# Performance work log

Hardware: AMD Instinct MI355X
Metric: run time of the kernel (lower is better)

The kernel has to match this reference:

```python
import jax, jax.numpy as jnp
import numpy as np

N_NODES = 50000
N_EDGES = 1000000
N_GRAPHS = 256
ORIG = 92
ATOM = 64
NBR = 41
EPS = 1e-5


def _bn_train(h, gamma, beta):
    # BatchNorm1d in training mode: batch stats, biased variance
    mu = h.mean(axis=0)
    var = jnp.var(h, axis=0)
    return (h - mu) * jax.lax.rsqrt(var + EPS) * gamma + beta


def setup_inputs() -> dict:
    key = jax.random.key(0)
    ks = jax.random.split(key, 16)
    inp = {
        "x": jax.random.normal(ks[0], (N_NODES, ORIG), dtype=jnp.float32),
        "edge_attr": jax.random.normal(ks[1], (N_EDGES, NBR), dtype=jnp.float32),
        "lower_f": jax.random.normal(ks[2], (N_NODES, ATOM), dtype=jnp.float32),
        "edge_index": jax.random.randint(ks[3], (2, N_EDGES), 0, N_NODES, dtype=jnp.int32),
        "batch": jnp.sort(jax.random.randint(ks[4], (N_NODES,), 0, N_GRAPHS, dtype=jnp.int32)),
        # params
        "emb_W": jax.random.normal(ks[5], (ORIG, ATOM), dtype=jnp.float32) / np.sqrt(ORIG),
        "emb_b": jnp.zeros((ATOM,), dtype=jnp.float32),
        "fc_W": jax.random.normal(ks[6], (2 * ATOM + NBR, 2 * ATOM), dtype=jnp.float32) / np.sqrt(2 * ATOM + NBR),
        "fc_b": jnp.zeros((2 * ATOM,), dtype=jnp.float32),
        "bn1_g": jnp.ones((2 * ATOM,), dtype=jnp.float32),
        "bn1_b": jnp.zeros((2 * ATOM,), dtype=jnp.float32),
        "bn2_g": jnp.ones((ATOM,), dtype=jnp.float32),
        "bn2_b": jnp.zeros((ATOM,), dtype=jnp.float32),
        "att_W": jax.random.normal(ks[7], (ATOM, 1), dtype=jnp.float32) / np.sqrt(ATOM),
        "att_b": jnp.zeros((1,), dtype=jnp.float32),
        "out_W": jax.random.normal(ks[8], (ATOM, 1), dtype=jnp.float32) / np.sqrt(ATOM),
        "out_b": jnp.zeros((1,), dtype=jnp.float32),
    }
    return inp


def reference(x, edge_attr, lower_f, emb_W, emb_b, fc_W, fc_b, bn1_g, bn1_b,
              bn2_g, bn2_b, att_W, att_b, out_W, out_b, edge_index, batch):
    # embedding + lower-level features
    atom_fea = x @ emb_W + emb_b + lower_f  # [N, ATOM]

    # CGConv: gather endpoints, concat with edge features
    src, dst = edge_index[0], edge_index[1]
    total = jnp.concatenate([atom_fea[src], atom_fea[dst], edge_attr], axis=-1)  # [E, 2A+NBR]
    gated = _bn_train(total @ fc_W + fc_b, bn1_g, bn1_b)  # [E, 2A]
    nbr_filter, nbr_core = gated[:, :ATOM], gated[:, ATOM:]
    msg = jax.nn.sigmoid(nbr_filter) * jax.nn.softplus(nbr_core)  # [E, A]
    summed = jax.ops.segment_sum(msg, src, num_segments=N_NODES)  # [N, A]
    atom_out = _bn_train(summed, bn2_g, bn2_b)

    # SiLU + attentional aggregation per graph
    h = jax.nn.silu(atom_out)  # [N, A]
    logits = (h @ att_W + att_b)[:, 0]  # [N]
    seg_max = jax.ops.segment_max(logits, batch, num_segments=N_GRAPHS)
    e = jnp.exp(logits - seg_max[batch])
    denom = jax.ops.segment_sum(e, batch, num_segments=N_GRAPHS)
    alpha = e / denom[batch]  # [N]
    crys = jax.ops.segment_sum(alpha[:, None] * h, batch, num_segments=N_GRAPHS)  # [G, A]
    crys_fea = crys @ out_W + out_b  # [G, 1]
    return atom_out, crys_fea
```

## Files before the change

kernel.cpp:

```cpp
#include <hip/hip_runtime.h>
#include <math.h>

#define NN 50000
#define NE 1000000
#define NG 256
#define ORIGD 92
#define NBRD 41
#define NSPREAD 32
#define SCAN_B 256

typedef unsigned short u16;
typedef __attribute__((ext_vector_type(8))) short short8;
typedef __attribute__((ext_vector_type(4))) float f32x4;

#define OFF_AFB     0
#define OFF_SUMMED  1600000
#define OFF_WT      4800000
#define OFF_BN1SPR  4812288
#define OFF_BN1SC   4820480
#define OFF_BN2ACC  4820736
#define OFF_BN2SC   4820864
#define OFF_ELOG    4820992
#define OFF_SEGMAX  4870992
#define OFF_DENOM   4871248
#define OFF_CRYS    4871504
#define OFF_CNT     4887888
#define OFF_PTR     4937888
#define OFF_HEAD    4987888
#define OFF_BSUM    5037888
#define OFF_BOFS    5038144
#define OFF_EIDX    5038400
#define OFF_H       6038400
#define OFF_BIG_END 70038400

__device__ __forceinline__ u16 f2b(float f) {
    unsigned u = __float_as_uint(f);
    return (u16)((u + 0x7FFFu + ((u >> 16) & 1u)) >> 16);
}
__device__ __forceinline__ float b2f(u16 u) {
    return __uint_as_float(((unsigned)u) << 16);
}

__global__ __launch_bounds__(256) void k_embed(
    const float* __restrict__ x, const float* __restrict__ lf,
    const float* __restrict__ W, const float* __restrict__ b,
    u16* __restrict__ afb)
{
    int gid = blockIdx.x * 256 + threadIdx.x;
    int n = gid >> 6, c = gid & 63;
    const float* xr = x + (long)n * ORIGD;
    float acc = b[c] + lf[gid];
#pragma unroll 4
    for (int k = 0; k < ORIGD; k++)
        acc = fmaf(xr[k], W[k * 64 + c], acc);
    afb[gid] = f2b(acc);
}

__global__ void k_prepw(const float* __restrict__ fcW, u16* __restrict__ wT)
{
    int i = blockIdx.x * 256 + threadIdx.x;
    int j = i / 192, k = i - j * 192;
    wT[i] = (k < 169) ? f2b(fcW[k * 128 + j]) : (u16)0;
}

__global__ void k_hist(const int* __restrict__ ei, int* __restrict__ cnt)
{
    int e = blockIdx.x * 256 + threadIdx.x;
    if (e < NE) atomicAdd(&cnt[ei[e]], 1);
}

__global__ void k_partial(const int* __restrict__ cnt, int* __restrict__ lofs,
                          int* __restrict__ bsum)
{
    __shared__ int sd[SCAN_B];
    int t = threadIdx.x, b = blockIdx.x, n = b * SCAN_B + t;
    int v = (n < NN) ? cnt[n] : 0;
    sd[t] = v; __syncthreads();
    for (int o = 1; o < SCAN_B; o <<= 1) {
        int x = (t >= o) ? sd[t - o] : 0;
        __syncthreads();
        sd[t] += x;
        __syncthreads();
    }
    if (n < NN) lofs[n] = sd[t] - v;
    if (t == SCAN_B - 1) bsum[b] = sd[t];
}

__global__ void k_scanb(const int* __restrict__ bsum, int* __restrict__ bofs, int nb)
{
    __shared__ int sd[256];
    int t = threadIdx.x;
    int v = (t < nb) ? bsum[t] : 0;
    sd[t] = v; __syncthreads();
    for (int o = 1; o < 256; o <<= 1) {
        int x = (t >= o) ? sd[t - o] : 0;
        __syncthreads();
        sd[t] += x;
        __syncthreads();
    }
    bofs[t] = sd[t] - v;
}

__global__ void k_addofs(int* __restrict__ ptr, const int* __restrict__ bofs,
                         int* __restrict__ head)
{
    int n = blockIdx.x * 256 + threadIdx.x;
    if (n < NN) {
        int p = ptr[n] + bofs[n >> 8];
        ptr[n] = p; head[n] = p;
    }
}

__global__ void k_fill(const int* __restrict__ ei, int* __restrict__ head,
                       int* __restrict__ eidx)
{
    int e = blockIdx.x * 256 + threadIdx.x;
    if (e < NE) {
        int pos = atomicAdd(&head[ei[e]], 1);
        eidx[pos] = e;
    }
}

__global__ __launch_bounds__(256) void k_gemm_h(
    const u16* __restrict__ afb, const float* __restrict__ ea,
    const int* __restrict__ ei, const u16* __restrict__ wT,
    u16* __restrict__ h, float* __restrict__ spread)
{
    __shared__ __align__(16) u16 sTl[64 * 200];
    __shared__ int sSrc[64], sDst[64];
    const int tid = threadIdx.x;
    const int e0 = blockIdx.x * 64;

    if (tid < 64) sSrc[tid] = ei[e0 + tid];
    else if (tid < 128) sDst[tid - 64] = ei[NE + e0 + tid - 64];
    __syncthreads();

    for (int i = tid; i < 1024; i += 256) {
        int e = i >> 4, q = i & 15;
        const u16* g = (q < 8) ? (afb + (long)sSrc[e] * 64 + q * 8)
                               : (afb + (long)sDst[e] * 64 + (q - 8) * 8);
        *(short8*)(sTl + e * 200 + q * 8) = *(const short8*)g;
    }
    for (int i = tid; i < 64 * 64; i += 256) {
        int e = i >> 6, c = i & 63;
        float v = (c < NBRD) ? ea[(long)(e0 + e) * NBRD + c] : 0.f;
        sTl[e * 200 + 128 + c] = f2b(v);
    }
    __syncthreads();

    const int lane = tid & 63, w = tid >> 6;
    const int n16 = lane & 15, quad = lane >> 4;

    short8 A0[6], A1[6];
    {
        const u16* b0 = wT + (16 * w + n16) * 192 + quad * 8;
        const u16* b1 = wT + (16 * (w + 4) + n16) * 192 + quad * 8;
#pragma unroll
        for (int ks = 0; ks < 6; ks++) {
            A0[ks] = *(const short8*)(b0 + ks * 32);
            A1[ks] = *(const short8*)(b1 + ks * 32);
        }
    }

    const int j0 = 16 * w + 4 * quad;
    float s0[4] = {0,0,0,0}, q0[4] = {0,0,0,0}, s1[4] = {0,0,0,0}, q1[4] = {0,0,0,0};

    for (int t = 0; t < 4; t++) {
        const u16* row = sTl + (16 * t + n16) * 200 + quad * 8;
        f32x4 acc0 = {0.f, 0.f, 0.f, 0.f}, acc1 = {0.f, 0.f, 0.f, 0.f};
#pragma unroll
        for (int ks = 0; ks < 6; ks++) {
            short8 b = *(const short8*)(row + ks * 32);
            acc0 = __builtin_amdgcn_mfma_f32_16x16x32_bf16(A0[ks], b, acc0, 0, 0, 0);
            acc1 = __builtin_amdgcn_mfma_f32_16x16x32_bf16(A1[ks], b, acc1, 0, 0, 0);
        }
#pragma unroll
        for (int r = 0; r < 4; r++) {
            s0[r] += acc0[r]; q0[r] = fmaf(acc0[r], acc0[r], q0[r]);
            s1[r] += acc1[r]; q1[r] = fmaf(acc1[r], acc1[r], q1[r]);
        }
        int ge = e0 + 16 * t + n16;
        u16* hp = h + (long)ge * 128 + j0;
        ushort4 v0 = make_ushort4(f2b(acc0[0]), f2b(acc0[1]), f2b(acc0[2]), f2b(acc0[3]));
        ushort4 v1 = make_ushort4(f2b(acc1[0]), f2b(acc1[1]), f2b(acc1[2]), f2b(acc1[3]));
        *(ushort4*)hp = v0;
        *(ushort4*)(hp + 64) = v1;
    }

#pragma unroll
    for (int m = 1; m < 16; m <<= 1) {
#pragma unroll
        for (int r = 0; r < 4; r++) {
            s0[r] += __shfl_xor(s0[r], m); q0[r] += __shfl_xor(q0[r], m);
            s1[r] += __shfl_xor(s1[r], m); q1[r] += __shfl_xor(q1[r], m);
        }
    }
    if (n16 == 0) {
        float* sp = spread + (blockIdx.x & (NSPREAD - 1)) * 256;
#pragma unroll
        for (int r = 0; r < 4; r++) {
            atomicAdd(sp + j0 + r,       s0[r]);
            atomicAdd(sp + 128 + j0 + r, q0[r]);
            atomicAdd(sp + 64 + j0 + r,  s1[r]);
            atomicAdd(sp + 192 + j0 + r, q1[r]);
        }
    }
}

template <int MODE>
__global__ __launch_bounds__(256) void k_gemm(
    const u16* __restrict__ afb, const float* __restrict__ ea,
    const int* __restrict__ ei, const u16* __restrict__ wT,
    const float* __restrict__ sc, float* __restrict__ outbuf)
{
    __shared__ __align__(16) u16 sTl[64 * 200];
    __shared__ int sSrc[64], sDst[64];
    const int tid = threadIdx.x;
    const int e0 = blockIdx.x * 64;

    if (tid < 64) sSrc[tid] = ei[e0 + tid];
    else if (tid < 128) sDst[tid - 64] = ei[NE + e0 + tid - 64];
    __syncthreads();
    for (int i = tid; i < 1024; i += 256) {
        int e = i >> 4, q = i & 15;
        const u16* g = (q < 8) ? (afb + (long)sSrc[e] * 64 + q * 8)
                               : (afb + (long)sDst[e] * 64 + (q - 8) * 8);
        *(short8*)(sTl + e * 200 + q * 8) = *(const short8*)g;
    }
    for (int i = tid; i < 64 * 64; i += 256) {
        int e = i >> 6, c = i & 63;
        float v = (c < NBRD) ? ea[(long)(e0 + e) * NBRD + c] : 0.f;
        sTl[e * 200 + 128 + c] = f2b(v);
    }
    __syncthreads();

    const int lane = tid & 63, w = tid >> 6;
    const int n16 = lane & 15, quad = lane >> 4;
    short8 A0[6], A1[6];
    {
        const u16* b0 = wT + (16 * w + n16) * 192 + quad * 8;
        const u16* b1 = wT + (16 * (w + 4) + n16) * 192 + quad * 8;
#pragma unroll
        for (int ks = 0; ks < 6; ks++) {
            A0[ks] = *(const short8*)(b0 + ks * 32);
            A1[ks] = *(const short8*)(b1 + ks * 32);
        }
    }
    const int j0 = 16 * w + 4 * quad;
    float s0[4] = {0,0,0,0}, q0[4] = {0,0,0,0}, s1[4] = {0,0,0,0}, q1[4] = {0,0,0,0};
    float scf[4], shf[4], scc[4], shc[4];
    if (MODE == 1) {
#pragma unroll
        for (int r = 0; r < 4; r++) {
            scf[r] = sc[j0 + r];        shf[r] = sc[128 + j0 + r];
            scc[r] = sc[64 + j0 + r];   shc[r] = sc[192 + j0 + r];
        }
    }
    for (int t = 0; t < 4; t++) {
        const u16* row = sTl + (16 * t + n16) * 200 + quad * 8;
        f32x4 acc0 = {0.f, 0.f, 0.f, 0.f}, acc1 = {0.f, 0.f, 0.f, 0.f};
#pragma unroll
        for (int ks = 0; ks < 6; ks++) {
            short8 b = *(const short8*)(row + ks * 32);
            acc0 = __builtin_amdgcn_mfma_f32_16x16x32_bf16(A0[ks], b, acc0, 0, 0, 0);
            acc1 = __builtin_amdgcn_mfma_f32_16x16x32_bf16(A1[ks], b, acc1, 0, 0, 0);
        }
        if (MODE == 0) {
#pragma unroll
            for (int r = 0; r < 4; r++) {
                s0[r] += acc0[r]; q0[r] = fmaf(acc0[r], acc0[r], q0[r]);
                s1[r] += acc1[r]; q1[r] = fmaf(acc1[r], acc1[r], q1[r]);
            }
        } else {
            int src = sSrc[16 * t + n16];
            float* dst = outbuf + (long)src * 64 + j0;
#pragma unroll
            for (int r = 0; r < 4; r++) {
                float f  = fmaf(acc0[r], scf[r], shf[r]);
                float cc = fmaf(acc1[r], scc[r], shc[r]);
                float sig = 1.f / (1.f + expf(-f));
                float sp  = fmaxf(cc, 0.f) + log1pf(expf(-fabsf(cc)));
                atomicAdd(dst + r, sig * sp);
            }
        }
    }
    if (MODE == 0) {
#pragma unroll
        for (int m = 1; m < 16; m <<= 1) {
#pragma unroll
            for (int r = 0; r < 4; r++) {
                s0[r] += __shfl_xor(s0[r], m); q0[r] += __shfl_xor(q0[r], m);
                s1[r] += __shfl_xor(s1[r], m); q1[r] += __shfl_xor(q1[r], m);
            }
        }
        if (n16 == 0) {
            float* sp = outbuf + (blockIdx.x & (NSPREAD - 1)) * 256;
#pragma unroll
            for (int r = 0; r < 4; r++) {
                atomicAdd(sp + j0 + r,       s0[r]);
                atomicAdd(sp + 128 + j0 + r, q0[r]);
                atomicAdd(sp + 64 + j0 + r,  s1[r]);
                atomicAdd(sp + 192 + j0 + r, q1[r]);
            }
        }
    }
}

__global__ void k_bn1fin(const float* __restrict__ spread,
                         const float* __restrict__ g, const float* __restrict__ b,
                         float* __restrict__ sc)
{
    int c = threadIdx.x;
    float s = 0.f, q = 0.f;
    for (int k = 0; k < NSPREAD; k++) { s += spread[k * 256 + c]; q += spread[k * 256 + 128 + c]; }
    float mean_acc = s / (float)NE;
    float var = q / (float)NE - mean_acc * mean_acc;
    float scale = g[c] * rsqrtf(var + 1e-5f);
    sc[c] = scale;
    sc[128 + c] = b[c] - mean_acc * scale;
}

__global__ __launch_bounds__(256) void k_scatter(
    const u16* __restrict__ h, const int* __restrict__ ptr,
    const int* __restrict__ cnt, const int* __restrict__ eidx,
    const float* __restrict__ sc, float* __restrict__ summed)
{
    int tid = threadIdx.x;
    int n = blockIdx.x * 4 + (tid >> 6);
    int l = tid & 63;
    float scf = sc[l],      shf = sc[128 + l];
    float scc = sc[64 + l], shc = sc[192 + l];
    int p0 = ptr[n], p1 = p0 + cnt[n];
    float acc = 0.f;
    int e_next = (p0 < p1) ? eidx[p0] : 0;
    for (int i = p0; i < p1; ) {
        int e = e_next;
        ++i;
        if (i < p1) e_next = eidx[i];
        const u16* hr = h + (long)e * 128;
        float f  = fmaf(b2f(hr[l]),      scf, shf);
        float cc = fmaf(b2f(hr[64 + l]), scc, shc);
        float sig = 1.f / (1.f + expf(-f));
        float sp  = fmaxf(cc, 0.f) + log1pf(expf(-fabsf(cc)));
        acc = fmaf(sig, sp, acc);
    }
    summed[(long)n * 64 + l] = acc;
}

__global__ __launch_bounds__(256) void k_bn2stats(const float* __restrict__ summed,
                                                  float* __restrict__ acc2)
{
    int tid = threadIdx.x; int c = tid & 63; int sub = tid >> 6;
    float s = 0.f, q = 0.f;
    for (int r = blockIdx.x * 4 + sub; r < NN; r += 4 * 128) {
        float v = summed[(long)r * 64 + c]; s += v; q = fmaf(v, v, q);
    }
    __shared__ float rs[256], rq[256];
    rs[tid] = s; rq[tid] = q; __syncthreads();
    if (tid < 64) {
        s = rs[tid] + rs[tid + 64] + rs[tid + 128] + rs[tid + 192];
        q = rq[tid] + rq[tid + 64] + rq[tid + 128] + rq[tid + 192];
        atomicAdd(&acc2[tid], s);
        atomicAdd(&acc2[64 + tid], q);
    }
}

__global__ void k_bn2fin(const float* __restrict__ acc2,
                         const float* __restrict__ g, const float* __restrict__ b,
                         float* __restrict__ sc2)
{
    int c = threadIdx.x;
    float mean = acc2[c] / (float)NN;
    float var = acc2[64 + c] / (float)NN - mean * mean;
    float scale = g[c] * rsqrtf(var + 1e-5f);
    sc2[c] = scale;
    sc2[64 + c] = b[c] - mean * scale;
}

__global__ __launch_bounds__(256) void k_nodepost(
    const float* __restrict__ summed, const float* __restrict__ sc2,
    const float* __restrict__ attW, const float* __restrict__ attb,
    const int* __restrict__ batch, float* __restrict__ out,
    float* __restrict__ elog, unsigned* __restrict__ segmax)
{
    int tid = threadIdx.x; int n = blockIdx.x * 4 + (tid >> 6); int c = tid & 63;
    float v = summed[(long)n * 64 + c];
    float ao = fmaf(v, sc2[c], sc2[64 + c]);
    out[(long)n * 64 + c] = ao;
    float h = ao / (1.f + expf(-ao));
    float p = h * attW[c];
#pragma unroll
    for (int off = 32; off; off >>= 1) p += __shfl_down(p, off, 64);
    if (c == 0) {
        float logit = p + attb[0];
        elog[n] = logit;
        unsigned u = __float_as_uint(logit);
        u = (u & 0x80000000u) ? ~u : (u | 0x80000000u);
        atomicMax(&segmax[batch[n]], u);
    }
}

__global__ void k_denom(const int* __restrict__ batch,
                        const unsigned* __restrict__ segmax,
                        float* __restrict__ elog, float* __restrict__ denom)
{
    int n = blockIdx.x * 256 + threadIdx.x;
    if (n >= NN) return;
    int b = batch[n];
    unsigned u = segmax[b];
    u = (u & 0x80000000u) ? (u & 0x7FFFFFFFu) : ~u;
    float e = expf(elog[n] - __uint_as_float(u));
    elog[n] = e;
    atomicAdd(&denom[b], e);
}

__global__ __launch_bounds__(256) void k_crys(
    const float* __restrict__ out, const float* __restrict__ elog,
    const float* __restrict__ denom, const int* __restrict__ batch,
    float* __restrict__ crys)
{
    int tid = threadIdx.x; int n = blockIdx.x * 4 + (tid >> 6); int c = tid & 63;
    int b = batch[n];
    float alpha = elog[n] / denom[b];
    float ao = out[(long)n * 64 + c];
    float h = ao / (1.f + expf(-ao));
    atomicAdd(&crys[b * 64 + c], alpha * h);
}

__global__ void k_final(const float* __restrict__ crys,
                        const float* __restrict__ outW, const float* __restrict__ outb,
                        float* __restrict__ out)
{
    int g = blockIdx.x; int c = threadIdx.x;
    float p = crys[g * 64 + c] * outW[c];
#pragma unroll
    for (int off = 32; off; off >>= 1) p += __shfl_down(p, off, 64);
    if (c == 0) out[(long)NN * 64 + g] = p + outb[0];
}

extern "C" void kernel_launch(void* const* d_in, const int* in_sizes, int n_in,
                              void* d_out, int out_size, void* d_ws, size_t ws_size,
                              hipStream_t stream)
{
    const float* x    = (const float*)d_in[0];
    const float* eatt = (const float*)d_in[1];
    const float* lf   = (const float*)d_in[2];
    const int*   ei   = (const int*)d_in[3];
    const int*   batch= (const int*)d_in[4];
    const float* embW = (const float*)d_in[5];
    const float* embB = (const float*)d_in[6];
    const float* fcW  = (const float*)d_in[7];
    const float* bn1g = (const float*)d_in[9];
    const float* bn1b = (const float*)d_in[10];
    const float* bn2g = (const float*)d_in[11];
    const float* bn2b = (const float*)d_in[12];
    const float* attW = (const float*)d_in[13];
    const float* attB = (const float*)d_in[14];
    const float* outW = (const float*)d_in[15];
    const float* outB = (const float*)d_in[16];
    float* out = (float*)d_out;
    float* ws  = (float*)d_ws;

    u16* afb = (u16*)(ws + OFF_AFB);
    u16* wT  = (u16*)(ws + OFF_WT);
    int* cnt  = (int*)(ws + OFF_CNT);
    int* ptr  = (int*)(ws + OFF_PTR);
    int* head = (int*)(ws + OFF_HEAD);
    int* bsum = (int*)(ws + OFF_BSUM);
    int* bofs = (int*)(ws + OFF_BOFS);
    int* eidx = (int*)(ws + OFF_EIDX);
    u16* h    = (u16*)(ws + OFF_H);

    const bool big = ws_size >= (size_t)OFF_BIG_END * sizeof(float);

    k_embed<<<12500, 256, 0, stream>>>(x, lf, embW, embB, afb);
    k_prepw<<<96, 256, 0, stream>>>(fcW, wT);

    if (big) {
        hipMemsetAsync(ws + OFF_BN1SPR, 0,
                       (size_t)(OFF_PTR - OFF_BN1SPR) * sizeof(float), stream);
        k_hist<<<(NE + 255) / 256, 256, 0, stream>>>(ei, cnt);
        k_partial<<<(NN + SCAN_B - 1) / SCAN_B, SCAN_B, 0, stream>>>(cnt, ptr, bsum);
        k_scanb<<<1, 256, 0, stream>>>(bsum, bofs, (NN + SCAN_B - 1) / SCAN_B);
        k_addofs<<<(NN + 255) / 256, 256, 0, stream>>>(ptr, bofs, head);
        k_fill<<<(NE + 255) / 256, 256, 0, stream>>>(ei, head, eidx);
        k_gemm_h<<<NE / 64, 256, 0, stream>>>(afb, eatt, ei, wT, h, ws + OFF_BN1SPR);
        k_bn1fin<<<1, 128, 0, stream>>>(ws + OFF_BN1SPR, bn1g, bn1b, ws + OFF_BN1SC);
        k_scatter<<<NN / 4, 256, 0, stream>>>(h, ptr, cnt, eidx, ws + OFF_BN1SC,
                                              ws + OFF_SUMMED);
    } else {
        hipMemsetAsync(ws + OFF_SUMMED, 0,
                       (size_t)(OFF_CNT - OFF_SUMMED) * sizeof(float), stream);
        k_gemm<0><<<NE / 64, 256, 0, stream>>>(afb, eatt, ei, wT, ws + OFF_BN1SC,
                                               ws + OFF_BN1SPR);
        k_bn1fin<<<1, 128, 0, stream>>>(ws + OFF_BN1SPR, bn1g, bn1b, ws + OFF_BN1SC);
        k_gemm<1><<<NE / 64, 256, 0, stream>>>(afb, eatt, ei, wT, ws + OFF_BN1SC,
                                               ws + OFF_SUMMED);
    }

    k_bn2stats<<<128, 256, 0, stream>>>(ws + OFF_SUMMED, ws + OFF_BN2ACC);
    k_bn2fin<<<1, 64, 0, stream>>>(ws + OFF_BN2ACC, bn2g, bn2b, ws + OFF_BN2SC);
    k_nodepost<<<12500, 256, 0, stream>>>(ws + OFF_SUMMED, ws + OFF_BN2SC, attW, attB, batch,
                                          out, ws + OFF_ELOG, (unsigned*)(ws + OFF_SEGMAX));
    k_denom<<<196, 256, 0, stream>>>(batch, (const unsigned*)(ws + OFF_SEGMAX),
                                     ws + OFF_ELOG, ws + OFF_DENOM);
    k_crys<<<12500, 256, 0, stream>>>(out, ws + OFF_ELOG, ws + OFF_DENOM, batch,
                                      ws + OFF_CRYS);
    k_final<<<NG, 64, 0, stream>>>(ws + OFF_CRYS, outW, outB, out);
}
```

Baseline: 1.272 ms.

## Write edge GEMM rows in CSR order and vectorize segment scatter

The edge GEMM now writes each output row directly to its sorted slot, computed per edge with an atomic on head. The scatter kernel can then read contiguous rows with 16-byte loads, spreading 8 edges by 8 channel-groups per wave and reducing with shuffles, instead of chasing an edge-index list. Edge attributes are also pre-converted to padded bf16 in a separate pass when workspace allows, and the final crystal projection is folded into k_crys with per-node atomics, which removes k_final and the crys buffer. The cost is an extra pre-pass over edge_attr, scattered row writes from the GEMM, and more atomics on the output.

```diff
diff --git a/kernel.cpp b/kernel.cpp
--- a/kernel.cpp
+++ b/kernel.cpp
@@ -23,15 +23,16 @@
 #define OFF_ELOG    4820992
 #define OFF_SEGMAX  4870992
 #define OFF_DENOM   4871248
-#define OFF_CRYS    4871504
-#define OFF_CNT     4887888
-#define OFF_PTR     4937888
-#define OFF_HEAD    4987888
-#define OFF_BSUM    5037888
-#define OFF_BOFS    5038144
-#define OFF_EIDX    5038400
-#define OFF_H       6038400
-#define OFF_BIG_END 70038400
+#define OFF_CNT     4871504
+#define OFF_PTR     4921504
+#define OFF_HEAD    4971504
+#define OFF_BSUM    5021504
+#define OFF_BOFS    5021760
+#define OFF_SLOT    5022016
+#define OFF_H       6022016
+#define OFF_T2_END  70022016
+#define OFF_EAB     70022016
+#define OFF_T3_END  94022016
 
 __device__ __forceinline__ u16 f2b(float f) {
     unsigned u = __float_as_uint(f);
@@ -61,6 +62,13 @@
     int i = blockIdx.x * 256 + threadIdx.x;
     int j = i / 192, k = i - j * 192;
     wT[i] = (k < 169) ? f2b(fcW[k * 128 + j]) : (u16)0;
+}
+
+__global__ void k_prepea(const float* __restrict__ ea, u16* __restrict__ eab)
+{
+    int gid = blockIdx.x * 256 + threadIdx.x;
+    int e = gid / 48, c = gid - e * 48;
+    eab[gid] = (c < NBRD) ? f2b(ea[(long)e * NBRD + c]) : (u16)0;
 }
 
 __global__ void k_hist(const int* __restrict__ ei, int* __restrict__ cnt)
@@ -111,28 +119,28 @@
     }
 }
 
-__global__ void k_fill(const int* __restrict__ ei, int* __restrict__ head,
-                       int* __restrict__ eidx)
+__global__ void k_slot(const int* __restrict__ ei, int* __restrict__ head,
+                       int* __restrict__ slot)
 {
     int e = blockIdx.x * 256 + threadIdx.x;
-    if (e < NE) {
-        int pos = atomicAdd(&head[ei[e]], 1);
-        eidx[pos] = e;
-    }
-}
-
+    if (e < NE) slot[e] = atomicAdd(&head[ei[e]], 1);
+}
+
+template <int EAB>
 __global__ __launch_bounds__(256) void k_gemm_h(
     const u16* __restrict__ afb, const float* __restrict__ ea,
-    const int* __restrict__ ei, const u16* __restrict__ wT,
+    const u16* __restrict__ eab, const int* __restrict__ ei,
+    const int* __restrict__ slot, const u16* __restrict__ wT,
     u16* __restrict__ h, float* __restrict__ spread)
 {
     __shared__ __align__(16) u16 sTl[64 * 200];
-    __shared__ int sSrc[64], sDst[64];
+    __shared__ int sSrc[64], sDst[64], sSlot[64];
     const int tid = threadIdx.x;
     const int e0 = blockIdx.x * 64;
 
     if (tid < 64) sSrc[tid] = ei[e0 + tid];
     else if (tid < 128) sDst[tid - 64] = ei[NE + e0 + tid - 64];
+    else if (tid < 192) sSlot[tid - 128] = slot[e0 + tid - 128];
     __syncthreads();
 
     for (int i = tid; i < 1024; i += 256) {
@@ -141,10 +149,24 @@
                                : (afb + (long)sDst[e] * 64 + (q - 8) * 8);
         *(short8*)(sTl + e * 200 + q * 8) = *(const short8*)g;
     }
-    for (int i = tid; i < 64 * 64; i += 256) {
-        int e = i >> 6, c = i & 63;
-        float v = (c < NBRD) ? ea[(long)(e0 + e) * NBRD + c] : 0.f;
-        sTl[e * 200 + 128 + c] = f2b(v);
+    if (EAB) {
+        for (int i = tid; i < 512; i += 256) {
+            if (i < 384) {
+                int e = i / 6, q = i - e * 6;
+                *(short8*)(sTl + e * 200 + 128 + q * 8) =
+                    *(const short8*)(eab + (long)(e0 + e) * 48 + q * 8);
+            } else {
+                int j = i - 384; int e = j >> 1, q = j & 1;
+                short8 z = {0,0,0,0,0,0,0,0};
+                *(short8*)(sTl + e * 200 + 176 + q * 8) = z;
+            }
+        }
+    } else {
+        for (int i = tid; i < 64 * 64; i += 256) {
+            int e = i >> 6, c = i & 63;
+            float v = (c < NBRD) ? ea[(long)(e0 + e) * NBRD + c] : 0.f;
+            sTl[e * 200 + 128 + c] = f2b(v);
+        }
     }
     __syncthreads();
 
@@ -179,8 +201,7 @@
             s0[r] += acc0[r]; q0[r] = fmaf(acc0[r], acc0[r], q0[r]);
             s1[r] += acc1[r]; q1[r] = fmaf(acc1[r], acc1[r], q1[r]);
         }
-        int ge = e0 + 16 * t + n16;
-        u16* hp = h + (long)ge * 128 + j0;
+        u16* hp = h + (long)sSlot[16 * t + n16] * 128 + j0;
         ushort4 v0 = make_ushort4(f2b(acc0[0]), f2b(acc0[1]), f2b(acc0[2]), f2b(acc0[3]));
         ushort4 v1 = make_ushort4(f2b(acc1[0]), f2b(acc1[1]), f2b(acc1[2]), f2b(acc1[3]));
         *(ushort4*)hp = v0;
@@ -322,29 +343,56 @@
 
 __global__ __launch_bounds__(256) void k_scatter(
     const u16* __restrict__ h, const int* __restrict__ ptr,
-    const int* __restrict__ cnt, const int* __restrict__ eidx,
-    const float* __restrict__ sc, float* __restrict__ summed)
+    const int* __restrict__ cnt, const float* __restrict__ sc,
+    float* __restrict__ summed)
 {
     int tid = threadIdx.x;
     int n = blockIdx.x * 4 + (tid >> 6);
     int l = tid & 63;
-    float scf = sc[l],      shf = sc[128 + l];
-    float scc = sc[64 + l], shc = sc[192 + l];
-    int p0 = ptr[n], p1 = p0 + cnt[n];
-    float acc = 0.f;
-    int e_next = (p0 < p1) ? eidx[p0] : 0;
-    for (int i = p0; i < p1; ) {
-        int e = e_next;
-        ++i;
-        if (i < p1) e_next = eidx[i];
-        const u16* hr = h + (long)e * 128;
-        float f  = fmaf(b2f(hr[l]),      scf, shf);
-        float cc = fmaf(b2f(hr[64 + l]), scc, shc);
-        float sig = 1.f / (1.f + expf(-f));
-        float sp  = fmaxf(cc, 0.f) + log1pf(expf(-fabsf(cc)));
-        acc = fmaf(sig, sp, acc);
-    }
-    summed[(long)n * 64 + l] = acc;
+    int es = l & 7, cg = l >> 3;
+
+    float4 a0 = *(const float4*)(sc + cg * 8);
+    float4 a1 = *(const float4*)(sc + cg * 8 + 4);
+    float4 b0 = *(const float4*)(sc + 128 + cg * 8);
+    float4 b1 = *(const float4*)(sc + 128 + cg * 8 + 4);
+    float4 c0 = *(const float4*)(sc + 64 + cg * 8);
+    float4 c1 = *(const float4*)(sc + 64 + cg * 8 + 4);
+    float4 d0 = *(const float4*)(sc + 192 + cg * 8);
+    float4 d1 = *(const float4*)(sc + 192 + cg * 8 + 4);
+    float scf[8] = {a0.x,a0.y,a0.z,a0.w,a1.x,a1.y,a1.z,a1.w};
+    float shf[8] = {b0.x,b0.y,b0.z,b0.w,b1.x,b1.y,b1.z,b1.w};
+    float scc[8] = {c0.x,c0.y,c0.z,c0.w,c1.x,c1.y,c1.z,c1.w};
+    float shc[8] = {d0.x,d0.y,d0.z,d0.w,d1.x,d1.y,d1.z,d1.w};
+
+    int p0 = ptr[n], deg = cnt[n];
+    float acc[8] = {0,0,0,0,0,0,0,0};
+    for (int i = 0; i < deg; i += 8) {
+        int idx = i + es;
+        bool valid = idx < deg;
+        long r = p0 + (valid ? idx : 0);
+        const u16* hr = h + r * 128;
+        short8 f8 = *(const short8*)(hr + cg * 8);
+        short8 c8 = *(const short8*)(hr + 64 + cg * 8);
+#pragma unroll
+        for (int j = 0; j < 8; j++) {
+            float f  = fmaf(b2f((u16)f8[j]), scf[j], shf[j]);
+            float cc = fmaf(b2f((u16)c8[j]), scc[j], shc[j]);
+            float sig = 1.f / (1.f + expf(-f));
+            float sp  = fmaxf(cc, 0.f) + log1pf(expf(-fabsf(cc)));
+            acc[j] += valid ? sig * sp : 0.f;
+        }
+    }
+#pragma unroll
+    for (int m = 1; m < 8; m <<= 1)
+#pragma unroll
+        for (int j = 0; j < 8; j++) acc[j] += __shfl_xor(acc[j], m);
+    if (es == 0) {
+        float* sp = summed + (long)n * 64 + cg * 8;
+        float4 v0 = {acc[0], acc[1], acc[2], acc[3]};
+        float4 v1 = {acc[4], acc[5], acc[6], acc[7]};
+        *(float4*)sp = v0;
+        *(float4*)(sp + 4) = v1;
+    }
 }
 
 __global__ __launch_bounds__(256) void k_bn2stats(const float* __restrict__ summed,
@@ -367,14 +415,18 @@
 
 __global__ void k_bn2fin(const float* __restrict__ acc2,
                          const float* __restrict__ g, const float* __restrict__ b,
-                         float* __restrict__ sc2)
+                         float* __restrict__ sc2, const float* __restrict__ outb,
+                         float* __restrict__ out)
 {
     int c = threadIdx.x;
-    float mean = acc2[c] / (float)NN;
-    float var = acc2[64 + c] / (float)NN - mean * mean;
-    float scale = g[c] * rsqrtf(var + 1e-5f);
-    sc2[c] = scale;
-    sc2[64 + c] = b[c] - mean * scale;
+    if (c < 64) {
+        float mean = acc2[c] / (float)NN;
+        float var = acc2[64 + c] / (float)NN - mean * mean;
+        float scale = g[c] * rsqrtf(var + 1e-5f);
+        sc2[c] = scale;
+        sc2[64 + c] = b[c] - mean * scale;
+    }
+    out[(long)NN * 64 + c] = outb[0];
 }
 
 __global__ __launch_bounds__(256) void k_nodepost(
@@ -415,27 +467,19 @@
 }
 
 __global__ __launch_bounds__(256) void k_crys(
-    const float* __restrict__ out, const float* __restrict__ elog,
+    const float* __restrict__ atom_out, const float* __restrict__ elog,
     const float* __restrict__ denom, const int* __restrict__ batch,
-    float* __restrict__ crys)
-{
-    int tid = threadIdx.x; int n = blockIdx.x * 4 + (tid >> 6); int c = tid & 63;
+    const float* __restrict__ outW, float* __restrict__ out)
+{
+    int tid = threadIdx.x; int n = blockIdx.x * 4 + (tid >> 6); int l = tid & 63;
     int b = batch[n];
     float alpha = elog[n] / denom[b];
-    float ao = out[(long)n * 64 + c];
+    float ao = atom_out[(long)n * 64 + l];
     float h = ao / (1.f + expf(-ao));
-    atomicAdd(&crys[b * 64 + c], alpha * h);
-}
-
-__global__ void k_final(const float* __restrict__ crys,
-                        const float* __restrict__ outW, const float* __restrict__ outb,
-                        float* __restrict__ out)
-{
-    int g = blockIdx.x; int c = threadIdx.x;
-    float p = crys[g * 64 + c] * outW[c];
+    float p = h * outW[l];
 #pragma unroll
     for (int off = 32; off; off >>= 1) p += __shfl_down(p, off, 64);
-    if (c == 0) out[(long)NN * 64 + g] = p + outb[0];
+    if (l == 0) atomicAdd(&out[(long)NN * 64 + b], alpha * p);
 }
 
 extern "C" void kernel_launch(void* const* d_in, const int* in_sizes, int n_in,
@@ -461,36 +505,44 @@
     float* out = (float*)d_out;
     float* ws  = (float*)d_ws;
 
-    u16* afb = (u16*)(ws + OFF_AFB);
-    u16* wT  = (u16*)(ws + OFF_WT);
+    u16* afb  = (u16*)(ws + OFF_AFB);
+    u16* wT   = (u16*)(ws + OFF_WT);
     int* cnt  = (int*)(ws + OFF_CNT);
     int* ptr  = (int*)(ws + OFF_PTR);
     int* head = (int*)(ws + OFF_HEAD);
     int* bsum = (int*)(ws + OFF_BSUM);
     int* bofs = (int*)(ws + OFF_BOFS);
-    int* eidx = (int*)(ws + OFF_EIDX);
+    int* slot = (int*)(ws + OFF_SLOT);
     u16* h    = (u16*)(ws + OFF_H);
-
-    const bool big = ws_size >= (size_t)OFF_BIG_END * sizeof(float);
+    u16* eab  = (u16*)(ws + OFF_EAB);
+
+    const bool t3 = ws_size >= (size_t)OFF_T3_END * sizeof(float);
+    const bool t2 = ws_size >= (size_t)OFF_T2_END * sizeof(float);
 
     k_embed<<<12500, 256, 0, stream>>>(x, lf, embW, embB, afb);
     k_prepw<<<96, 256, 0, stream>>>(fcW, wT);
 
-    if (big) {
+    if (t2) {
         hipMemsetAsync(ws + OFF_BN1SPR, 0,
                        (size_t)(OFF_PTR - OFF_BN1SPR) * sizeof(float), stream);
+        if (t3) k_prepea<<<NE * 48 / 256, 256, 0, stream>>>(eatt, eab);
         k_hist<<<(NE + 255) / 256, 256, 0, stream>>>(ei, cnt);
         k_partial<<<(NN + SCAN_B - 1) / SCAN_B, SCAN_B, 0, stream>>>(cnt, ptr, bsum);
         k_scanb<<<1, 256, 0, stream>>>(bsum, bofs, (NN + SCAN_B - 1) / SCAN_B);
         k_addofs<<<(NN + 255) / 256, 256, 0, stream>>>(ptr, bofs, head);
-        k_fill<<<(NE + 255) / 256, 256, 0, stream>>>(ei, head, eidx);
-        k_gemm_h<<<NE / 64, 256, 0, stream>>>(afb, eatt, ei, wT, h, ws + OFF_BN1SPR);
+        k_slot<<<(NE + 255) / 256, 256, 0, stream>>>(ei, head, slot);
+        if (t3)
+            k_gemm_h<1><<<NE / 64, 256, 0, stream>>>(afb, eatt, eab, ei, slot, wT,
+                                                     h, ws + OFF_BN1SPR);
+        else
+            k_gemm_h<0><<<NE / 64, 256, 0, stream>>>(afb, eatt, eab, ei, slot, wT,
+                                                     h, ws + OFF_BN1SPR);
         k_bn1fin<<<1, 128, 0, stream>>>(ws + OFF_BN1SPR, bn1g, bn1b, ws + OFF_BN1SC);
-        k_scatter<<<NN / 4, 256, 0, stream>>>(h, ptr, cnt, eidx, ws + OFF_BN1SC,
+        k_scatter<<<NN / 4, 256, 0, stream>>>(h, ptr, cnt, ws + OFF_BN1SC,
                                               ws + OFF_SUMMED);
     } else {
         hipMemsetAsync(ws + OFF_SUMMED, 0,
-                       (size_t)(OFF_CNT - OFF_SUMMED) * sizeof(float), stream);
+                       (size_t)(OFF_PTR - OFF_SUMMED) * sizeof(float), stream);
         k_gemm<0><<<NE / 64, 256, 0, stream>>>(afb, eatt, ei, wT, ws + OFF_BN1SC,
                                                ws + OFF_BN1SPR);
         k_bn1fin<<<1, 128, 0, stream>>>(ws + OFF_BN1SPR, bn1g, bn1b, ws + OFF_BN1SC);
@@ -499,12 +551,13 @@
     }
 
     k_bn2stats<<<128, 256, 0, stream>>>(ws + OFF_SUMMED, ws + OFF_BN2ACC);
-    k_bn2fin<<<1, 64, 0, stream>>>(ws + OFF_BN2ACC, bn2g, bn2b, ws + OFF_BN2SC);
-    k_nodepost<<<12500, 256, 0, stream>>>(ws + OFF_SUMMED, ws + OFF_BN2SC, attW, attB, batch,
-                                          out, ws + OFF_ELOG, (unsigned*)(ws + OFF_SEGMAX));
+    k_bn2fin<<<1, 256, 0, stream>>>(ws + OFF_BN2ACC, bn2g, bn2b, ws + OFF_BN2SC,
+                                    outB, out);
+    k_nodepost<<<12500, 256, 0, stream>>>(ws + OFF_SUMMED, ws + OFF_BN2SC, attW, attB,
+                                          batch, out, ws + OFF_ELOG,
+                                          (unsigned*)(ws + OFF_SEGMAX));
     k_denom<<<196, 256, 0, stream>>>(batch, (const unsigned*)(ws + OFF_SEGMAX),
                                      ws + OFF_ELOG, ws + OFF_DENOM);
     k_crys<<<12500, 256, 0, stream>>>(out, ws + OFF_ELOG, ws + OFF_DENOM, batch,
-                                      ws + OFF_CRYS);
-    k_final<<<NG, 64, 0, stream>>>(ws + OFF_CRYS, outW, outB, out);
-}
+                                      outW, out);
+}
```

New measurement: 1.396 ms. +9.7%, slower.
